# Kernel tuning notes

Measured on AMD Instinct MI355X. Metric: run time of the kernel, lower is better.

## Reference

```python
import jax, jax.numpy as jnp
import numpy as np

S, B, H = 2048, 16, 512      # seq_len, batch, hidden_size
L = 4096                     # total labels across batch
SMAX = 16                    # max span length
LAB = 256                    # label_size
V = 32000                    # len(voc)


def setup_inputs() -> dict:
    key = jax.random.key(0)
    ks = jax.random.split(key, 10)
    hidden = jax.random.normal(ks[0], (S, B, H), jnp.float32)
    begins = jax.random.randint(ks[1], (L,), 1, S - SMAX - 1)          # >=1 so begin-1 valid
    lens = jax.random.randint(ks[2], (L,), 1, SMAX + 1)                # span length in [1, SMAX]
    ends = begins + lens                                               # < S so hidden[end] valid
    bids = jax.random.randint(ks[3], (L,), 0, B)
    tags = jax.random.randint(ks[4], (L,), 0, V)
    sc = 0.02
    W1 = jax.random.normal(ks[5], (3 * H, LAB), jnp.float32) * sc
    b1 = jnp.zeros((LAB,), jnp.float32)
    W2 = jax.random.normal(ks[6], (LAB, LAB), jnp.float32) * sc
    b2 = jnp.zeros((LAB,), jnp.float32)
    Wo = jax.random.normal(ks[7], (LAB, V), jnp.float32) * sc
    bo = jnp.zeros((V,), jnp.float32)
    return dict(hidden=hidden, begins=begins, ends=ends, bids=bids, tags=tags,
                W1=W1, b1=b1, W2=W2, b2=b2, Wo=Wo, bo=bo)


def reference(hidden, begins, ends, bids, tags, W1, b1, W2, b2, Wo, bo):
    # --- batched span embed: gather + masked mean + boundary concat ---
    pos = begins[:, None] + jnp.arange(SMAX)            # [L, SMAX]
    valid = (pos < ends[:, None]).astype(hidden.dtype)  # [L, SMAX]
    posc = jnp.minimum(pos, S - 1)
    g = hidden[posc, bids[:, None]]                     # [L, SMAX, H] gather
    span_len = (ends - begins).astype(hidden.dtype)[:, None]
    mean = (g * valid[..., None]).sum(axis=1) / span_len           # [L, H]
    left = hidden[begins - 1, bids]                                 # [L, H]
    right = hidden[ends, bids]                                      # [L, H]
    span_emb = jnp.concatenate([left, mean, right], axis=-1)        # [L, 3H]
    # --- hidden2feature: Linear -> sigmoid -> Linear (dropout = eval identity) ---
    feat = jax.nn.sigmoid(span_emb @ W1 + b1) @ W2 + b2             # [L, LAB]
    # --- SoftmaxLoss: -log_softmax(h2o(feat)).gather(tags).mean() per label ---
    logp = jax.nn.log_softmax(feat @ Wo + bo, axis=-1)              # [L, V]
    per_label = -logp[jnp.arange(L), tags]                          # one tag per label
    return per_label.sum() / (L + 1e-5)
```

## Files before the change

### kernel.cpp

```cpp
#include <hip/hip_runtime.h>
#include <math.h>

#define S 2048
#define B 16
#define H 512
#define L 4096
#define SMAX 16
#define LAB 256
#define V 32000
#define NCH 250
#define LOG2E 1.44269504f

typedef __attribute__((ext_vector_type(8))) short short8;
typedef __attribute__((ext_vector_type(4))) float float4v;

__device__ inline ushort f2bf(float x) {
  union { float f; unsigned u; } c; c.f = x;
  unsigned r = c.u + 0x7fffu + ((c.u >> 16) & 1u);
  return (ushort)(r >> 16);
}
__device__ inline float bf2f(ushort h) {
  union { unsigned u; float f; } c; c.u = ((unsigned)h) << 16;
  return c.f;
}

__global__ __launch_bounds__(256) void spanb_kernel(
    const float* __restrict__ hidden, const int* __restrict__ begins,
    const int* __restrict__ ends, const int* __restrict__ bids,
    ushort* __restrict__ spanb) {
  int sub = threadIdx.x >> 7, t = threadIdx.x & 127;
  int l = blockIdx.x * 2 + sub;
  int b = bids[l], s0 = begins[l], s1 = ends[l];
  const float4* hidv = (const float4*)hidden;
  float4 lf = hidv[((size_t)(s0 - 1) * B + b) * 128 + t];
  float4 rf = hidv[((size_t)s1 * B + b) * 128 + t];
  float4 m = make_float4(0.f, 0.f, 0.f, 0.f);
  int len = s1 - s0;
  for (int j = 0; j < len; ++j) {
    float4 g = hidv[((size_t)(s0 + j) * B + b) * 128 + t];
    m.x += g.x; m.y += g.y; m.z += g.z; m.w += g.w;
  }
  float inv = 1.0f / (float)len;
  ushort* sp = spanb + (size_t)l * 1536;
  ushort4 u;
  u.x = f2bf(lf.x); u.y = f2bf(lf.y); u.z = f2bf(lf.z); u.w = f2bf(lf.w);
  *(ushort4*)&sp[t * 4] = u;
  u.x = f2bf(m.x * inv); u.y = f2bf(m.y * inv);
  u.z = f2bf(m.z * inv); u.w = f2bf(m.w * inv);
  *(ushort4*)&sp[512 + t * 4] = u;
  u.x = f2bf(rf.x); u.y = f2bf(rf.y); u.z = f2bf(rf.z); u.w = f2bf(rf.w);
  *(ushort4*)&sp[1024 + t * 4] = u;
}

__global__ __launch_bounds__(256) void tcast_kernel(
    const float* __restrict__ src, ushort* __restrict__ dst, int K, int N) {
  __shared__ ushort tile[64 * 72];
  int t = threadIdx.x;
  int n0 = blockIdx.x * 64;
  int k0 = blockIdx.y * 64;
  #pragma unroll
  for (int p = 0; p < 16; ++p) {
    int k = p * 4 + (t >> 6);
    int n = t & 63;
    tile[n * 72 + k] = f2bf(src[(size_t)(k0 + k) * N + n0 + n]);
  }
  __syncthreads();
  #pragma unroll
  for (int p = 0; p < 2; ++p) {
    int idx = p * 256 + t;
    int n = idx >> 3, c = idx & 7;
    *(uint4*)&dst[(size_t)(n0 + n) * K + k0 + c * 8] =
        *(const uint4*)&tile[n * 72 + c * 8];
  }
}

__global__ __launch_bounds__(256) void tcast_wo_kernel(
    const float* __restrict__ src, ushort* __restrict__ dst) {
  __shared__ ushort tile[64 * 72];
  int t = threadIdx.x;
  int n0 = blockIdx.x * 64;
  int k0 = blockIdx.y * 64;
  #pragma unroll
  for (int p = 0; p < 16; ++p) {
    int k = p * 4 + (t >> 6);
    int n = t & 63;
    tile[n * 72 + k] = f2bf(src[(size_t)(k0 + k) * V + n0 + n]);
  }
  __syncthreads();
  #pragma unroll
  for (int p = 0; p < 2; ++p) {
    int idx = p * 256 + t;
    int n = idx >> 3, c8 = idx & 7;
    int v = n0 + n, k = k0 + c8 * 8;
    int c = v >> 7, nt = (v >> 4) & 7, lr = v & 15;
    int kh = k >> 7, k4 = (k >> 5) & 3, lq = (k >> 3) & 3;
    size_t f = ((((size_t)c * 2 + kh) * 4 + k4) * 8 + nt) * 64 + lq * 16 + lr;
    *(uint4*)&dst[f * 8] = *(const uint4*)&tile[n * 72 + c8 * 8];
  }
}

#define FST 72
__global__ __launch_bounds__(256, 2) void feat_mfma_kernel(
    const ushort* __restrict__ spanb, const ushort* __restrict__ W1b,
    const float* __restrict__ b1, const ushort* __restrict__ W2b,
    const float* __restrict__ b2, ushort* __restrict__ featb) {
  __shared__ ushort As[32 * FST];
  __shared__ ushort Bs[256 * FST];
  __shared__ ushort Hs[32 * 264];
  int tid = threadIdx.x;
  int w = tid >> 6, lane = tid & 63;
  int lr = lane & 15, lq = lane >> 4;
  int l0 = blockIdx.x * 32;

  float4v acc[2][4];
  float4v zero = {0.f, 0.f, 0.f, 0.f};
  #pragma unroll
  for (int mt = 0; mt < 2; ++mt)
    #pragma unroll
    for (int nt = 0; nt < 4; ++nt) acc[mt][nt] = zero;

  for (int s = 0; s < 24; ++s) {
    int ks = s * 64;
    __syncthreads();
    {
      int r = tid >> 3, c = tid & 7;
      *(uint4*)&As[r * FST + c * 8] =
          *(const uint4*)&spanb[(size_t)(l0 + r) * 1536 + ks + c * 8];
    }
    #pragma unroll
    for (int p = 0; p < 8; ++p) {
      int idx = p * 256 + tid;
      int r = idx >> 3, c = idx & 7;
      *(uint4*)&Bs[r * FST + c * 8] =
          *(const uint4*)&W1b[(size_t)r * 1536 + ks + c * 8];
    }
    __syncthreads();
    #pragma unroll
    for (int kk = 0; kk < 2; ++kk) {
      short8 af[2], bf[4];
      #pragma unroll
      for (int mt = 0; mt < 2; ++mt)
        af[mt] = *(const short8*)&As[(mt * 16 + lr) * FST + kk * 32 + lq * 8];
      #pragma unroll
      for (int nt = 0; nt < 4; ++nt)
        bf[nt] = *(const short8*)
            &Bs[(w * 64 + nt * 16 + lr) * FST + kk * 32 + lq * 8];
      #pragma unroll
      for (int mt = 0; mt < 2; ++mt)
        #pragma unroll
        for (int nt = 0; nt < 4; ++nt)
          acc[mt][nt] = __builtin_amdgcn_mfma_f32_16x16x32_bf16(
              af[mt], bf[nt], acc[mt][nt], 0, 0, 0);
    }
  }

  {
    float b1v[4];
    #pragma unroll
    for (int nt = 0; nt < 4; ++nt) b1v[nt] = b1[w * 64 + nt * 16 + lr];
    #pragma unroll
    for (int mt = 0; mt < 2; ++mt)
      #pragma unroll
      for (int nt = 0; nt < 4; ++nt)
        #pragma unroll
        for (int r = 0; r < 4; ++r) {
          int row = mt * 16 + lq * 4 + r;
          int col = w * 64 + nt * 16 + lr;
          float h = 1.0f / (1.0f + __expf(-(acc[mt][nt][r] + b1v[nt])));
          Hs[row * 264 + col] = f2bf(h);
        }
  }

  float4v acc2[2][4];
  #pragma unroll
  for (int mt = 0; mt < 2; ++mt)
    #pragma unroll
    for (int nt = 0; nt < 4; ++nt) acc2[mt][nt] = zero;

  for (int s = 0; s < 4; ++s) {
    int ks = s * 64;
    __syncthreads();
    #pragma unroll
    for (int p = 0; p < 8; ++p) {
      int idx = p * 256 + tid;
      int r = idx >> 3, c = idx & 7;
      *(uint4*)&Bs[r * FST + c * 8] =
          *(const uint4*)&W2b[(size_t)r * 256 + ks + c * 8];
    }
    __syncthreads();
    #pragma unroll
    for (int kk = 0; kk < 2; ++kk) {
      short8 af[2], bf[4];
      #pragma unroll
      for (int mt = 0; mt < 2; ++mt)
        af[mt] = *(const short8*)
            &Hs[(mt * 16 + lr) * 264 + ks + kk * 32 + lq * 8];
      #pragma unroll
      for (int nt = 0; nt < 4; ++nt)
        bf[nt] = *(const short8*)
            &Bs[(w * 64 + nt * 16 + lr) * FST + kk * 32 + lq * 8];
      #pragma unroll
      for (int mt = 0; mt < 2; ++mt)
        #pragma unroll
        for (int nt = 0; nt < 4; ++nt)
          acc2[mt][nt] = __builtin_amdgcn_mfma_f32_16x16x32_bf16(
              af[mt], bf[nt], acc2[mt][nt], 0, 0, 0);
    }
  }

  {
    float b2v[4];
    #pragma unroll
    for (int nt = 0; nt < 4; ++nt) b2v[nt] = b2[w * 64 + nt * 16 + lr];
    #pragma unroll
    for (int mt = 0; mt < 2; ++mt)
      #pragma unroll
      for (int nt = 0; nt < 4; ++nt)
        #pragma unroll
        for (int r = 0; r < 4; ++r) {
          int row = mt * 16 + lq * 4 + r;
          int col = w * 64 + nt * 16 + lr;
          featb[(size_t)(l0 + row) * 256 + col] =
              f2bf(acc2[mt][nt][r] + b2v[nt]);
        }
  }
}

__global__ __launch_bounds__(256, 3) void logits2_kernel(
    const ushort* __restrict__ featb, const ushort* __restrict__ Wob,
    const float* __restrict__ bo, float* __restrict__ pz) {
  __shared__ ushort Blds[16384];
  int tid = threadIdx.x;
  int w = tid >> 6, lane = tid & 63;
  int lr = lane & 15, lq = lane >> 4;
  int l0 = blockIdx.x * 128;
  int v0 = blockIdx.y * 128;

  const short8* aptr[2];
  #pragma unroll
  for (int mt = 0; mt < 2; ++mt)
    aptr[mt] = (const short8*)(featb +
        (size_t)(l0 + w * 32 + mt * 16 + lr) * 256 + lq * 8);

  float bov[8];
  #pragma unroll
  for (int nt = 0; nt < 8; ++nt)
    bov[nt] = bo[v0 + nt * 16 + lr] * LOG2E;

  float4v acc[2][8];
  float4v zero = {0.f, 0.f, 0.f, 0.f};
  #pragma unroll
  for (int mt = 0; mt < 2; ++mt)
    #pragma unroll
    for (int nt = 0; nt < 8; ++nt) acc[mt][nt] = zero;

  short8 af[2][2];
  #pragma unroll
  for (int mt = 0; mt < 2; ++mt) af[0][mt] = aptr[mt][0];

  #pragma unroll
  for (int kh = 0; kh < 2; ++kh) {
    {
      const uint4* src4 = (const uint4*)(Wob +
          (size_t)blockIdx.y * 32768 + (size_t)kh * 16384);
      #pragma unroll
      for (int p = 0; p < 8; ++p) {
        int idx = p * 256 + tid;
        __builtin_amdgcn_global_load_lds(
            (const __attribute__((address_space(1))) unsigned int*)(src4 + idx),
            (__attribute__((address_space(3))) unsigned int*)&Blds[(size_t)idx * 8],
            16, 0, 0);
      }
    }
    __syncthreads();
    #pragma unroll
    for (int k4 = 0; k4 < 4; ++k4) {
      int kg = kh * 4 + k4;
      int cur = kg & 1, nxt = cur ^ 1;
      if (kg < 7) {
        #pragma unroll
        for (int mt = 0; mt < 2; ++mt)
          af[nxt][mt] = aptr[mt][(kg + 1) * 4];
      }
      short8 bf[8];
      #pragma unroll
      for (int nt = 0; nt < 8; ++nt)
        bf[nt] = *(const short8*)&Blds[(size_t)(((k4 * 8 + nt) * 64) + lane) * 8];
      __builtin_amdgcn_s_setprio(1);
      #pragma unroll
      for (int mt = 0; mt < 2; ++mt)
        #pragma unroll
        for (int nt = 0; nt < 8; ++nt)
          acc[mt][nt] = __builtin_amdgcn_mfma_f32_16x16x32_bf16(
              af[cur][mt], bf[nt], acc[mt][nt], 0, 0, 0);
      __builtin_amdgcn_s_setprio(0);
    }
    if (kh == 0) __syncthreads();
  }

  float z[2][4];
  #pragma unroll
  for (int mt = 0; mt < 2; ++mt)
    #pragma unroll
    for (int r = 0; r < 4; ++r) z[mt][r] = 0.f;
  #pragma unroll
  for (int mt = 0; mt < 2; ++mt)
    #pragma unroll
    for (int nt = 0; nt < 8; ++nt)
      #pragma unroll
      for (int r = 0; r < 4; ++r)
        z[mt][r] += exp2f(fmaf(acc[mt][nt][r], LOG2E, bov[nt]));
  #pragma unroll
  for (int mt = 0; mt < 2; ++mt)
    #pragma unroll
    for (int r = 0; r < 4; ++r) {
      #pragma unroll
      for (int off = 1; off < 16; off <<= 1)
        z[mt][r] += __shfl_xor(z[mt][r], off);
    }
  if (lr == 0) {
    int ch = blockIdx.y;
    #pragma unroll
    for (int mt = 0; mt < 2; ++mt) {
      float4 v4;
      v4.x = z[mt][0]; v4.y = z[mt][1]; v4.z = z[mt][2]; v4.w = z[mt][3];
      *(float4*)&pz[(size_t)ch * L + l0 + w * 32 + mt * 16 + lq * 4] = v4;
    }
  }
}

__global__ __launch_bounds__(256) void tag_kernel(
    const ushort* __restrict__ featb, const ushort* __restrict__ Wob,
    const float* __restrict__ bo, const int* __restrict__ tags,
    float* __restrict__ tagl) {
  int l = blockIdx.x * 4 + (threadIdx.x >> 6);
  int lane = threadIdx.x & 63;
  int tg = tags[l];
  int c = tg >> 7, nt = (tg >> 4) & 7, lr = tg & 15;
  int k0 = lane << 2;
  int kh = k0 >> 7, k4 = (k0 >> 5) & 3, lq = (k0 >> 3) & 3, e = k0 & 7;
  size_t f = ((((size_t)c * 2 + kh) * 4 + k4) * 8 + nt) * 64 + lq * 16 + lr;
  ushort4 wa = *(const ushort4*)&Wob[f * 8 + e];
  ushort4 fa = *(const ushort4*)&featb[(size_t)l * 256 + k0];
  float s = bf2f(fa.x) * bf2f(wa.x) + bf2f(fa.y) * bf2f(wa.y) +
            bf2f(fa.z) * bf2f(wa.z) + bf2f(fa.w) * bf2f(wa.w);
  #pragma unroll
  for (int off = 1; off < 64; off <<= 1) s += __shfl_xor(s, off);
  if (lane == 0) tagl[l] = s + bo[tg];
}

__global__ __launch_bounds__(256) void reduce_kernel(
    const float* __restrict__ pz, const float* __restrict__ tagl,
    float* __restrict__ out) {
  int l = blockIdx.x * 256 + threadIdx.x;
  float z = 0.f;
  for (int c = 0; c < NCH; ++c) z += pz[(size_t)c * L + l];
  float per = logf(z) - tagl[l];
  float v = per * (1.0f / (4096.0f + 1e-5f));
  #pragma unroll
  for (int off = 1; off < 64; off <<= 1) v += __shfl_xor(v, off);
  __shared__ float wsum[4];
  if ((threadIdx.x & 63) == 0) wsum[threadIdx.x >> 6] = v;
  __syncthreads();
  if (threadIdx.x == 0)
    atomicAdd(out, wsum[0] + wsum[1] + wsum[2] + wsum[3]);
}

extern "C" void kernel_launch(void* const* d_in, const int* in_sizes, int n_in,
                              void* d_out, int out_size, void* d_ws,
                              size_t ws_size, hipStream_t stream) {
  const float* hidden = (const float*)d_in[0];
  const int* begins = (const int*)d_in[1];
  const int* ends = (const int*)d_in[2];
  const int* bids = (const int*)d_in[3];
  const int* tags = (const int*)d_in[4];
  const float* W1 = (const float*)d_in[5];
  const float* b1 = (const float*)d_in[6];
  const float* W2 = (const float*)d_in[7];
  const float* b2 = (const float*)d_in[8];
  const float* Wo = (const float*)d_in[9];
  const float* bo = (const float*)d_in[10];
  float* out = (float*)d_out;

  ushort* featb = (ushort*)d_ws;
  ushort* Wob = featb + (size_t)L * 256;
  ushort* spanb = Wob + (size_t)V * 256;
  ushort* W1b = spanb + (size_t)L * 1536;
  ushort* W2b = W1b + (size_t)256 * 1536;
  float* pz = (float*)spanb;
  float* tagl = (float*)(W2b + (size_t)256 * 256);

  hipMemsetAsync(d_out, 0, sizeof(float), stream);
  spanb_kernel<<<L / 2, 256, 0, stream>>>(hidden, begins, ends, bids, spanb);
  tcast_kernel<<<dim3(4, 24), 256, 0, stream>>>(W1, W1b, 1536, LAB);
  tcast_kernel<<<dim3(4, 4), 256, 0, stream>>>(W2, W2b, LAB, LAB);
  tcast_wo_kernel<<<dim3(500, 4), 256, 0, stream>>>(Wo, Wob);
  feat_mfma_kernel<<<128, 256, 0, stream>>>(spanb, W1b, b1, W2b, b2, featb);
  logits2_kernel<<<dim3(32, NCH), 256, 0, stream>>>(featb, Wob, bo, pz);
  tag_kernel<<<L / 4, 256, 0, stream>>>(featb, Wob, bo, tags, tagl);
  reduce_kernel<<<L / 256, 256, 0, stream>>>(pz, tagl, out);
}
```

Before: 290.4 us.

## Enlarge logits tile to 256 rows and load full K of Wo into LDS once

After: 353.3 us. +21.7%, slower.

```diff
diff --git a/kernel.cpp b/kernel.cpp
--- a/kernel.cpp
+++ b/kernel.cpp
@@ -226,92 +226,88 @@
   }
 }
 
-__global__ __launch_bounds__(256, 3) void logits2_kernel(
+__global__ __launch_bounds__(256, 2) void logits2_kernel(
     const ushort* __restrict__ featb, const ushort* __restrict__ Wob,
     const float* __restrict__ bo, float* __restrict__ pz) {
-  __shared__ ushort Blds[16384];
+  __shared__ ushort Blds[32768];
   int tid = threadIdx.x;
-  int w = tid >> 6, lane = tid & 63;
+  int lane = tid & 63;
+  int wl = tid >> 7;
+  int wv = (tid >> 6) & 1;
   int lr = lane & 15, lq = lane >> 4;
-  int l0 = blockIdx.x * 128;
+  int l0 = blockIdx.x * 256;
   int v0 = blockIdx.y * 128;
 
-  const short8* aptr[2];
-  #pragma unroll
-  for (int mt = 0; mt < 2; ++mt)
-    aptr[mt] = (const short8*)(featb +
-        (size_t)(l0 + w * 32 + mt * 16 + lr) * 256 + lq * 8);
-
-  float bov[8];
-  #pragma unroll
-  for (int nt = 0; nt < 8; ++nt)
-    bov[nt] = bo[v0 + nt * 16 + lr] * LOG2E;
-
-  float4v acc[2][8];
+  const short8* abase = (const short8*)(featb +
+      (size_t)(l0 + wl * 128 + lr) * 256 + lq * 8);
+
+  short8 af[2][8];
+  #pragma unroll
+  for (int mt = 0; mt < 8; ++mt) af[0][mt] = abase[mt * 512];
+
+  {
+    const uint4* src4 = (const uint4*)(Wob + (size_t)blockIdx.y * 32768);
+    #pragma unroll
+    for (int p = 0; p < 16; ++p) {
+      int idx = p * 256 + tid;
+      __builtin_amdgcn_global_load_lds(
+          (const __attribute__((address_space(1))) unsigned int*)(src4 + idx),
+          (__attribute__((address_space(3))) unsigned int*)&Blds[idx * 8],
+          16, 0, 0);
+    }
+  }
+
+  float4v acc[8][4];
   float4v zero = {0.f, 0.f, 0.f, 0.f};
   #pragma unroll
-  for (int mt = 0; mt < 2; ++mt)
-    #pragma unroll
-    for (int nt = 0; nt < 8; ++nt) acc[mt][nt] = zero;
-
-  short8 af[2][2];
-  #pragma unroll
-  for (int mt = 0; mt < 2; ++mt) af[0][mt] = aptr[mt][0];
-
-  #pragma unroll
-  for (int kh = 0; kh < 2; ++kh) {
-    {
-      const uint4* src4 = (const uint4*)(Wob +
-          (size_t)blockIdx.y * 32768 + (size_t)kh * 16384);
-      #pragma unroll
-      for (int p = 0; p < 8; ++p) {
-        int idx = p * 256 + tid;
-        __builtin_amdgcn_global_load_lds(
-            (const __attribute__((address_space(1))) unsigned int*)(src4 + idx),
-            (__attribute__((address_space(3))) unsigned int*)&Blds[(size_t)idx * 8],
-            16, 0, 0);
-      }
-    }
-    __syncthreads();
-    #pragma unroll
-    for (int k4 = 0; k4 < 4; ++k4) {
-      int kg = kh * 4 + k4;
-      int cur = kg & 1, nxt = cur ^ 1;
-      if (kg < 7) {
-        #pragma unroll
-        for (int mt = 0; mt < 2; ++mt)
-          af[nxt][mt] = aptr[mt][(kg + 1) * 4];
-      }
-      short8 bf[8];
-      #pragma unroll
-      for (int nt = 0; nt < 8; ++nt)
-        bf[nt] = *(const short8*)&Blds[(size_t)(((k4 * 8 + nt) * 64) + lane) * 8];
-      __builtin_amdgcn_s_setprio(1);
-      #pragma unroll
-      for (int mt = 0; mt < 2; ++mt)
-        #pragma unroll
-        for (int nt = 0; nt < 8; ++nt)
-          acc[mt][nt] = __builtin_amdgcn_mfma_f32_16x16x32_bf16(
-              af[cur][mt], bf[nt], acc[mt][nt], 0, 0, 0);
-      __builtin_amdgcn_s_setprio(0);
-    }
-    if (kh == 0) __syncthreads();
-  }
-
-  float z[2][4];
-  #pragma unroll
-  for (int mt = 0; mt < 2; ++mt)
+  for (int mt = 0; mt < 8; ++mt)
+    #pragma unroll
+    for (int nt = 0; nt < 4; ++nt) acc[mt][nt] = zero;
+
+  __syncthreads();
+
+  const ushort* bbase = &Blds[(wv * 4 * 64 + lane) * 8];
+
+  #pragma unroll
+  for (int kg = 0; kg < 8; ++kg) {
+    int cur = kg & 1, nxt = cur ^ 1;
+    if (kg < 7) {
+      #pragma unroll
+      for (int mt = 0; mt < 8; ++mt)
+        af[nxt][mt] = abase[mt * 512 + (kg + 1) * 4];
+    }
+    short8 bf[4];
+    #pragma unroll
+    for (int nt = 0; nt < 4; ++nt)
+      bf[nt] = *(const short8*)&bbase[kg * 4096 + nt * 512];
+    __builtin_amdgcn_s_setprio(1);
+    #pragma unroll
+    for (int mt = 0; mt < 8; ++mt)
+      #pragma unroll
+      for (int nt = 0; nt < 4; ++nt)
+        acc[mt][nt] = __builtin_amdgcn_mfma_f32_16x16x32_bf16(
+            af[cur][mt], bf[nt], acc[mt][nt], 0, 0, 0);
+    __builtin_amdgcn_s_setprio(0);
+  }
+
+  float bov[4];
+  #pragma unroll
+  for (int nt = 0; nt < 4; ++nt)
+    bov[nt] = bo[v0 + wv * 64 + nt * 16 + lr] * LOG2E;
+  float z[8][4];
+  #pragma unroll
+  for (int mt = 0; mt < 8; ++mt)
     #pragma unroll
     for (int r = 0; r < 4; ++r) z[mt][r] = 0.f;
   #pragma unroll
-  for (int mt = 0; mt < 2; ++mt)
-    #pragma unroll
-    for (int nt = 0; nt < 8; ++nt)
+  for (int mt = 0; mt < 8; ++mt)
+    #pragma unroll
+    for (int nt = 0; nt < 4; ++nt)
       #pragma unroll
       for (int r = 0; r < 4; ++r)
         z[mt][r] += exp2f(fmaf(acc[mt][nt][r], LOG2E, bov[nt]));
   #pragma unroll
-  for (int mt = 0; mt < 2; ++mt)
+  for (int mt = 0; mt < 8; ++mt)
     #pragma unroll
     for (int r = 0; r < 4; ++r) {
       #pragma unroll
@@ -319,12 +315,12 @@
         z[mt][r] += __shfl_xor(z[mt][r], off);
     }
   if (lr == 0) {
-    int ch = blockIdx.y;
-    #pragma unroll
-    for (int mt = 0; mt < 2; ++mt) {
+    int slot = blockIdx.y * 2 + wv;
+    #pragma unroll
+    for (int mt = 0; mt < 8; ++mt) {
       float4 v4;
       v4.x = z[mt][0]; v4.y = z[mt][1]; v4.z = z[mt][2]; v4.w = z[mt][3];
-      *(float4*)&pz[(size_t)ch * L + l0 + w * 32 + mt * 16 + lq * 4] = v4;
+      *(float4*)&pz[(size_t)slot * L + l0 + wl * 128 + mt * 16 + lq * 4] = v4;
     }
   }
 }
@@ -354,7 +350,7 @@
     float* __restrict__ out) {
   int l = blockIdx.x * 256 + threadIdx.x;
   float z = 0.f;
-  for (int c = 0; c < NCH; ++c) z += pz[(size_t)c * L + l];
+  for (int c = 0; c < 2 * NCH; ++c) z += pz[(size_t)c * L + l];
   float per = logf(z) - tagl[l];
   float v = per * (1.0f / (4096.0f + 1e-5f));
   #pragma unroll
@@ -396,7 +392,7 @@
   tcast_kernel<<<dim3(4, 4), 256, 0, stream>>>(W2, W2b, LAB, LAB);
   tcast_wo_kernel<<<dim3(500, 4), 256, 0, stream>>>(Wo, Wob);
   feat_mfma_kernel<<<128, 256, 0, stream>>>(spanb, W1b, b1, W2b, b2, featb);
-  logits2_kernel<<<dim3(32, NCH), 256, 0, stream>>>(featb, Wob, bo, pz);
+  logits2_kernel<<<dim3(16, NCH), 256, 0, stream>>>(featb, Wob, bo, pz);
   tag_kernel<<<L / 4, 256, 0, stream>>>(featb, Wob, bo, tags, tagl);
   reduce_kernel<<<L / 256, 256, 0, stream>>>(pz, tagl, out);
 }
```

## Restructure feature MLP kernel to stream operands from global memory with more blocks

Applied to the files above, without the earlier changes.

New measurement: 289.7 us. No clear change (-0.2%).

```diff
diff --git a/kernel.cpp b/kernel.cpp
--- a/kernel.cpp
+++ b/kernel.cpp
@@ -99,134 +99,102 @@
   }
 }
 
-#define FST 72
-__global__ __launch_bounds__(256, 2) void feat_mfma_kernel(
+__global__ __launch_bounds__(256) void feat_mfma_kernel(
     const ushort* __restrict__ spanb, const ushort* __restrict__ W1b,
     const float* __restrict__ b1, const ushort* __restrict__ W2b,
     const float* __restrict__ b2, ushort* __restrict__ featb) {
-  __shared__ ushort As[32 * FST];
-  __shared__ ushort Bs[256 * FST];
-  __shared__ ushort Hs[32 * 264];
+  __shared__ ushort Hs[16 * 264];
   int tid = threadIdx.x;
   int w = tid >> 6, lane = tid & 63;
   int lr = lane & 15, lq = lane >> 4;
-  int l0 = blockIdx.x * 32;
-
-  float4v acc[2][4];
+  int l0 = blockIdx.x * 16;
+
+  const short8* arow = (const short8*)(spanb + (size_t)(l0 + lr) * 1536 + lq * 8);
+  const short8* brow[4];
+  #pragma unroll
+  for (int nt = 0; nt < 4; ++nt)
+    brow[nt] = (const short8*)(W1b + (size_t)(w * 64 + nt * 16 + lr) * 1536 + lq * 8);
+
+  float4v acc[4];
   float4v zero = {0.f, 0.f, 0.f, 0.f};
   #pragma unroll
-  for (int mt = 0; mt < 2; ++mt)
-    #pragma unroll
-    for (int nt = 0; nt < 4; ++nt) acc[mt][nt] = zero;
-
-  for (int s = 0; s < 24; ++s) {
-    int ks = s * 64;
-    __syncthreads();
-    {
-      int r = tid >> 3, c = tid & 7;
-      *(uint4*)&As[r * FST + c * 8] =
-          *(const uint4*)&spanb[(size_t)(l0 + r) * 1536 + ks + c * 8];
-    }
-    #pragma unroll
-    for (int p = 0; p < 8; ++p) {
-      int idx = p * 256 + tid;
-      int r = idx >> 3, c = idx & 7;
-      *(uint4*)&Bs[r * FST + c * 8] =
-          *(const uint4*)&W1b[(size_t)r * 1536 + ks + c * 8];
-    }
-    __syncthreads();
-    #pragma unroll
-    for (int kk = 0; kk < 2; ++kk) {
-      short8 af[2], bf[4];
-      #pragma unroll
-      for (int mt = 0; mt < 2; ++mt)
-        af[mt] = *(const short8*)&As[(mt * 16 + lr) * FST + kk * 32 + lq * 8];
-      #pragma unroll
-      for (int nt = 0; nt < 4; ++nt)
-        bf[nt] = *(const short8*)
-            &Bs[(w * 64 + nt * 16 + lr) * FST + kk * 32 + lq * 8];
-      #pragma unroll
-      for (int mt = 0; mt < 2; ++mt)
-        #pragma unroll
-        for (int nt = 0; nt < 4; ++nt)
-          acc[mt][nt] = __builtin_amdgcn_mfma_f32_16x16x32_bf16(
-              af[mt], bf[nt], acc[mt][nt], 0, 0, 0);
-    }
+  for (int nt = 0; nt < 4; ++nt) acc[nt] = zero;
+
+  short8 af[2], bf[2][4];
+  af[0] = arow[0];
+  #pragma unroll
+  for (int nt = 0; nt < 4; ++nt) bf[0][nt] = brow[nt][0];
+
+  #pragma unroll
+  for (int s = 0; s < 48; ++s) {
+    int cur = s & 1, nxt = cur ^ 1;
+    if (s < 47) {
+      af[nxt] = arow[(s + 1) * 4];
+      #pragma unroll
+      for (int nt = 0; nt < 4; ++nt) bf[nxt][nt] = brow[nt][(s + 1) * 4];
+    }
+    #pragma unroll
+    for (int nt = 0; nt < 4; ++nt)
+      acc[nt] = __builtin_amdgcn_mfma_f32_16x16x32_bf16(
+          af[cur], bf[cur][nt], acc[nt], 0, 0, 0);
   }
 
   {
-    float b1v[4];
-    #pragma unroll
-    for (int nt = 0; nt < 4; ++nt) b1v[nt] = b1[w * 64 + nt * 16 + lr];
-    #pragma unroll
-    for (int mt = 0; mt < 2; ++mt)
-      #pragma unroll
-      for (int nt = 0; nt < 4; ++nt)
-        #pragma unroll
-        for (int r = 0; r < 4; ++r) {
-          int row = mt * 16 + lq * 4 + r;
-          int col = w * 64 + nt * 16 + lr;
-          float h = 1.0f / (1.0f + __expf(-(acc[mt][nt][r] + b1v[nt])));
-          Hs[row * 264 + col] = f2bf(h);
-        }
-  }
-
-  float4v acc2[2][4];
-  #pragma unroll
-  for (int mt = 0; mt < 2; ++mt)
-    #pragma unroll
-    for (int nt = 0; nt < 4; ++nt) acc2[mt][nt] = zero;
-
-  for (int s = 0; s < 4; ++s) {
-    int ks = s * 64;
-    __syncthreads();
-    #pragma unroll
-    for (int p = 0; p < 8; ++p) {
-      int idx = p * 256 + tid;
-      int r = idx >> 3, c = idx & 7;
-      *(uint4*)&Bs[r * FST + c * 8] =
-          *(const uint4*)&W2b[(size_t)r * 256 + ks + c * 8];
-    }
-    __syncthreads();
-    #pragma unroll
-    for (int kk = 0; kk < 2; ++kk) {
-      short8 af[2], bf[4];
-      #pragma unroll
-      for (int mt = 0; mt < 2; ++mt)
-        af[mt] = *(const short8*)
-            &Hs[(mt * 16 + lr) * 264 + ks + kk * 32 + lq * 8];
-      #pragma unroll
-      for (int nt = 0; nt < 4; ++nt)
-        bf[nt] = *(const short8*)
-            &Bs[(w * 64 + nt * 16 + lr) * FST + kk * 32 + lq * 8];
-      #pragma unroll
-      for (int mt = 0; mt < 2; ++mt)
-        #pragma unroll
-        for (int nt = 0; nt < 4; ++nt)
-          acc2[mt][nt] = __builtin_amdgcn_mfma_f32_16x16x32_bf16(
-              af[mt], bf[nt], acc2[mt][nt], 0, 0, 0);
-    }
+    #pragma unroll
+    for (int nt = 0; nt < 4; ++nt) {
+      float b1v = b1[w * 64 + nt * 16 + lr];
+      #pragma unroll
+      for (int r = 0; r < 4; ++r) {
+        int row = lq * 4 + r;
+        float h = 1.0f / (1.0f + __expf(-(acc[nt][r] + b1v)));
+        Hs[row * 264 + w * 64 + nt * 16 + lr] = f2bf(h);
+      }
+    }
+  }
+  __syncthreads();
+
+  const short8* wrow[4];
+  #pragma unroll
+  for (int nt = 0; nt < 4; ++nt)
+    wrow[nt] = (const short8*)(W2b + (size_t)(w * 64 + nt * 16 + lr) * 256 + lq * 8);
+
+  float4v acc2[4];
+  #pragma unroll
+  for (int nt = 0; nt < 4; ++nt) acc2[nt] = zero;
+
+  short8 bf2[2][4];
+  #pragma unroll
+  for (int nt = 0; nt < 4; ++nt) bf2[0][nt] = wrow[nt][0];
+
+  #pragma unroll
+  for (int s = 0; s < 8; ++s) {
+    int cur = s & 1, nxt = cur ^ 1;
+    if (s < 7) {
+      #pragma unroll
+      for (int nt = 0; nt < 4; ++nt) bf2[nxt][nt] = wrow[nt][(s + 1) * 4];
+    }
+    short8 af2 = *(const short8*)&Hs[lr * 264 + s * 32 + lq * 8];
+    #pragma unroll
+    for (int nt = 0; nt < 4; ++nt)
+      acc2[nt] = __builtin_amdgcn_mfma_f32_16x16x32_bf16(
+          af2, bf2[cur][nt], acc2[nt], 0, 0, 0);
   }
 
   {
-    float b2v[4];
-    #pragma unroll
-    for (int nt = 0; nt < 4; ++nt) b2v[nt] = b2[w * 64 + nt * 16 + lr];
-    #pragma unroll
-    for (int mt = 0; mt < 2; ++mt)
-      #pragma unroll
-      for (int nt = 0; nt < 4; ++nt)
-        #pragma unroll
-        for (int r = 0; r < 4; ++r) {
-          int row = mt * 16 + lq * 4 + r;
-          int col = w * 64 + nt * 16 + lr;
-          featb[(size_t)(l0 + row) * 256 + col] =
-              f2bf(acc2[mt][nt][r] + b2v[nt]);
-        }
-  }
-}
-
-__global__ __launch_bounds__(256, 3) void logits2_kernel(
+    #pragma unroll
+    for (int nt = 0; nt < 4; ++nt) {
+      float b2v = b2[w * 64 + nt * 16 + lr];
+      #pragma unroll
+      for (int r = 0; r < 4; ++r) {
+        int row = lq * 4 + r;
+        int col = w * 64 + nt * 16 + lr;
+        featb[(size_t)(l0 + row) * 256 + col] = f2bf(acc2[nt][r] + b2v);
+      }
+    }
+  }
+}
+
+__global__ __launch_bounds__(256, 4) void logits2_kernel(
     const ushort* __restrict__ featb, const ushort* __restrict__ Wob,
     const float* __restrict__ bo, float* __restrict__ pz) {
   __shared__ ushort Blds[16384];
@@ -241,11 +209,6 @@
   for (int mt = 0; mt < 2; ++mt)
     aptr[mt] = (const short8*)(featb +
         (size_t)(l0 + w * 32 + mt * 16 + lr) * 256 + lq * 8);
-
-  float bov[8];
-  #pragma unroll
-  for (int nt = 0; nt < 8; ++nt)
-    bov[nt] = bo[v0 + nt * 16 + lr] * LOG2E;
 
   float4v acc[2][8];
   float4v zero = {0.f, 0.f, 0.f, 0.f};
@@ -298,6 +261,10 @@
     if (kh == 0) __syncthreads();
   }
 
+  float bov[8];
+  #pragma unroll
+  for (int nt = 0; nt < 8; ++nt)
+    bov[nt] = bo[v0 + nt * 16 + lr] * LOG2E;
   float z[2][4];
   #pragma unroll
   for (int mt = 0; mt < 2; ++mt)
@@ -395,7 +362,7 @@
   tcast_kernel<<<dim3(4, 24), 256, 0, stream>>>(W1, W1b, 1536, LAB);
   tcast_kernel<<<dim3(4, 4), 256, 0, stream>>>(W2, W2b, LAB, LAB);
   tcast_wo_kernel<<<dim3(500, 4), 256, 0, stream>>>(Wo, Wob);
-  feat_mfma_kernel<<<128, 256, 0, stream>>>(spanb, W1b, b1, W2b, b2, featb);
+  feat_mfma_kernel<<<256, 256, 0, stream>>>(spanb, W1b, b1, W2b, b2, featb);
   logits2_kernel<<<dim3(32, NCH), 256, 0, stream>>>(featb, Wob, bo, pz);
   tag_kernel<<<L / 4, 256, 0, stream>>>(featb, Wob, bo, tags, tagl);
   reduce_kernel<<<L / 256, 256, 0, stream>>>(pz, tagl, out);
```
